# Kernel tuning notes

Hardware: AMD Instinct MI355X
Metric: run time of the kernel (lower is better)

## Reference

```python
import jax, jax.numpy as jnp
import numpy as np

B, T, C = 4, 2048, 1024
H = 16
HS = C // H  # 64
FF = 4 * C  # 4096


def setup_inputs() -> dict:
    key = jax.random.key(0)
    ks = jax.random.split(key, 10)
    s_in = C ** -0.5
    s_ff = FF ** -0.5
    return {
        "x": jax.random.normal(ks[0], (B, T, C), dtype=jnp.float32),
        "Wq": jax.random.normal(ks[1], (H, C, HS), dtype=jnp.float32) * s_in,
        "Wk": jax.random.normal(ks[2], (H, C, HS), dtype=jnp.float32) * s_in,
        "Wv": jax.random.normal(ks[3], (H, C, HS), dtype=jnp.float32) * s_in,
        "Wproj": jax.random.normal(ks[4], (C, C), dtype=jnp.float32) * s_in,
        "bproj": jax.random.normal(ks[5], (C,), dtype=jnp.float32) * 0.01,
        "W1": jax.random.normal(ks[6], (C, FF), dtype=jnp.float32) * s_in,
        "b1": jax.random.normal(ks[7], (FF,), dtype=jnp.float32) * 0.01,
        "W2": jax.random.normal(ks[8], (FF, C), dtype=jnp.float32) * s_ff,
        "b2": jax.random.normal(ks[9], (C,), dtype=jnp.float32) * 0.01,
    }


def reference(x, Wq, Wk, Wv, Wproj, bproj, W1, b1, W2, b2):
    b, t, c = x.shape
    # per-head projections, batched over heads: [B,H,T,HS]
    q = jnp.einsum("btc,hcd->bhtd", x, Wq)
    k = jnp.einsum("btc,hcd->bhtd", x, Wk)
    v = jnp.einsum("btc,hcd->bhtd", x, Wv)
    # NOTE: original scales by full embed dim c**-0.5, not head_size
    scores = jnp.einsum("bhtd,bhsd->bhts", q, k) * (c ** -0.5)
    causal = jnp.tril(jnp.ones((t, t), dtype=bool))
    scores = jnp.where(causal[None, None], scores, -jnp.inf)
    w = jax.nn.softmax(scores, axis=-1)
    y = jnp.einsum("bhts,bhsd->bhtd", w, v)  # [B,H,T,HS]
    y = jnp.transpose(y, (0, 2, 1, 3)).reshape(b, t, c)  # concat heads
    attn_out = y @ Wproj + bproj
    x = attn_out + x
    ff = jax.nn.relu(x @ W1 + b1) @ W2 + b2
    return ff + x
```

## Files before the change

### kernel.cpp

```cpp
#include <hip/hip_runtime.h>

typedef unsigned short u16;
typedef __attribute__((ext_vector_type(4))) float f32x4;
typedef __attribute__((ext_vector_type(8))) short bf16x8;

constexpr int kB  = 4;
constexpr int kT  = 2048;
constexpr int kC  = 1024;
constexpr int kH  = 16;
constexpr int kFF = 4096;
constexpr int kM  = kB * kT;
constexpr int k3C = 3 * kC;

__device__ __forceinline__ float b2f(u16 u) {
    union { unsigned int i; float f; } v;
    v.i = ((unsigned int)u) << 16;
    return v.f;
}
__device__ __forceinline__ u16 f2b(float f) {
    union { float f; unsigned int i; } v;
    v.f = f;
    unsigned int r = (v.i + 0x7FFFu + ((v.i >> 16) & 1u)) >> 16;
    return (u16)r;
}

__device__ __forceinline__ void lds_barrier() {
    __asm__ __volatile__("" ::: "memory");
    __builtin_amdgcn_s_waitcnt(0xC07F);
    __builtin_amdgcn_s_barrier();
    __asm__ __volatile__("" ::: "memory");
}

__global__ void cvt_f32_bf16(const float* __restrict__ in, u16* __restrict__ out, int n4)
{
    const int i = blockIdx.x * 256 + threadIdx.x;
    if (i >= n4) return;
    float4 v = *(const float4*)(in + (size_t)i * 4);
    ushort4 o;
    o.x = f2b(v.x); o.y = f2b(v.y); o.z = f2b(v.z); o.w = f2b(v.w);
    *(ushort4*)(out + (size_t)i * 4) = o;
}

__global__ void transpose_cvt(const float* __restrict__ in, int R, int Cc,
                              u16* __restrict__ out)
{
    __shared__ float t[32][33];
    const int bx = blockIdx.x * 32;
    const int by = blockIdx.y * 32;
    const int lx = threadIdx.x, ly = threadIdx.y;
    #pragma unroll
    for (int i = 0; i < 32; i += 8)
        t[ly + i][lx] = in[(size_t)(by + ly + i) * Cc + bx + lx];
    __syncthreads();
    #pragma unroll
    for (int i = 0; i < 32; i += 8)
        out[(size_t)(bx + ly + i) * R + by + lx] = f2b(t[lx][ly + i]);
}

__global__ void repack_qkv_t(const float* __restrict__ Wq, const float* __restrict__ Wk,
                             const float* __restrict__ Wv, u16* __restrict__ out)
{
    __shared__ float t[32][33];
    const int z = blockIdx.z;
    const int s = z >> 4, h = z & 15;
    const float* in = (s == 0 ? Wq : s == 1 ? Wk : Wv) + (size_t)h * (kC * 64);
    const int bx = blockIdx.x * 32;
    const int by = blockIdx.y * 32;
    const int lx = threadIdx.x, ly = threadIdx.y;
    #pragma unroll
    for (int i = 0; i < 32; i += 8)
        t[ly + i][lx] = in[(size_t)(by + ly + i) * 64 + bx + lx];
    __syncthreads();
    const int orow = s * kC + h * 64 + bx;
    #pragma unroll
    for (int i = 0; i < 32; i += 8)
        out[(size_t)(orow + ly + i) * kC + by + lx] = f2b(t[lx][ly + i]);
}

__global__ __launch_bounds__(256) void gemm_bt_mfma(
    const u16* __restrict__ A, int lda,
    const u16* __restrict__ Bt, int ldb,
    int K,
    const float* __restrict__ bias,
    const u16* __restrict__ resid,
    float* __restrict__ CoF,
    u16* __restrict__ CoB,
    int ldc, int do_relu)
{
    constexpr int BK = 64;
    __shared__ u16 As[128 * BK];
    __shared__ u16 Bs[128 * BK];
    const int tid  = threadIdx.x;
    const int wave = tid >> 6, lane = tid & 63;
    const int wm = (wave >> 1) * 64, wn = (wave & 1) * 64;
    const int m0 = blockIdx.y * 128, n0 = blockIdx.x * 128;

    const int srow = wave * 32;
    const int lrow = lane >> 3;
    const int scol = ((lane & 7) ^ lrow) * 8;

    const int fm   = lane & 15;
    const int fkq  = lane >> 4;

    f32x4 acc[4][4];
    #pragma unroll
    for (int i = 0; i < 4; ++i)
        #pragma unroll
        for (int j = 0; j < 4; ++j)
            acc[i][j] = (f32x4){0.f, 0.f, 0.f, 0.f};

    for (int k0 = 0; k0 < K; k0 += BK) {
        #pragma unroll
        for (int i = 0; i < 4; ++i) {
            const int r = srow + i * 8;
            const u16* ga = A  + (size_t)(m0 + r + lrow) * lda + k0 + scol;
            const u16* gb = Bt + (size_t)(n0 + r + lrow) * ldb + k0 + scol;
            __builtin_amdgcn_global_load_lds(
                (const __attribute__((address_space(1))) void*)ga,
                (__attribute__((address_space(3))) void*)&As[r * BK], 16, 0, 0);
            __builtin_amdgcn_global_load_lds(
                (const __attribute__((address_space(1))) void*)gb,
                (__attribute__((address_space(3))) void*)&Bs[r * BK], 16, 0, 0);
        }
        __syncthreads();
        #pragma unroll
        for (int ks = 0; ks < 2; ++ks) {
            bf16x8 a[4], b[4];
            #pragma unroll
            for (int i = 0; i < 4; ++i) {
                const int m = wm + i * 16 + fm;
                const int ck = ((ks * 4 + fkq) ^ (m & 7)) * 8;
                a[i] = *(const bf16x8*)&As[m * BK + ck];
            }
            #pragma unroll
            for (int j = 0; j < 4; ++j) {
                const int n = wn + j * 16 + fm;
                const int ck = ((ks * 4 + fkq) ^ (n & 7)) * 8;
                b[j] = *(const bf16x8*)&Bs[n * BK + ck];
            }
            #pragma unroll
            for (int i = 0; i < 4; ++i)
                #pragma unroll
                for (int j = 0; j < 4; ++j)
                    acc[i][j] = __builtin_amdgcn_mfma_f32_16x16x32_bf16(
                        a[i], b[j], acc[i][j], 0, 0, 0);
        }
        __syncthreads();
    }

    const int col = lane & 15;
    const int rb  = (lane >> 4) * 4;
    #pragma unroll
    for (int i = 0; i < 4; ++i) {
        #pragma unroll
        for (int j = 0; j < 4; ++j) {
            const int n = n0 + wn + j * 16 + col;
            #pragma unroll
            for (int r = 0; r < 4; ++r) {
                const int m = m0 + wm + i * 16 + rb + r;
                float v = acc[i][j][r];
                if (bias)    v += bias[n];
                if (do_relu) v = fmaxf(v, 0.f);
                if (resid)   v += b2f(resid[(size_t)m * ldc + n]);
                if (CoF) CoF[(size_t)m * ldc + n] = v;
                else     CoB[(size_t)m * ldc + n] = f2b(v);
            }
        }
    }
}

__global__ __launch_bounds__(256) void attn_mfma3(
    const u16* __restrict__ QKV, u16* __restrict__ Y)
{
    __shared__ __align__(16) u16 Kl[2][64 * 64];
    __shared__ __align__(16) u16 Vt[2][64 * 64];
    __shared__ __align__(16) u16 Pl[4][16 * 64];

    const int tid  = threadIdx.x;
    const int wave = tid >> 6, lane = tid & 63;
    const int ln = lane & 15, quad = lane >> 4;
    const int idx = blockIdx.x;
    const int bh = idx & 63;
    const int qt = 15 - (idx >> 6);
    const int b = bh >> 4, h = bh & 15;
    const int q0 = qt << 7;
    const int bT = b * kT;
    const int qgw = q0 + wave * 32;
    const float scale = 0.03125f;

    const u16* kvbase = QKV + (size_t)bT * k3C + kC + h * 64;

    const int sK = tid >> 3, cK = tid & 7;
    const int sV = (tid >> 3) * 2, cV = tid & 7;
    const int kwa0 = (sK << 6) + ((cK ^ (sK & 7)) << 3);
    const int kwa1 = kwa0 + (32 << 6);

    bf16x8 qa[2][2];
    #pragma unroll
    for (int qsub = 0; qsub < 2; ++qsub) {
        const size_t qb = ((size_t)bT + qgw + 16 * qsub + ln) * k3C + h * 64;
        qa[qsub][0] = *(const bf16x8*)(QKV + qb + quad * 8);
        qa[qsub][1] = *(const bf16x8*)(QKV + qb + 32 + quad * 8);
    }

    f32x4 acco[2][4];
    #pragma unroll
    for (int qsub = 0; qsub < 2; ++qsub)
        #pragma unroll
        for (int jd = 0; jd < 4; ++jd) acco[qsub][jd] = (f32x4){0.f, 0.f, 0.f, 0.f};
    float mrun[2] = {-1e30f, -1e30f}, lrun[2] = {0.f, 0.f};
    u16* Pw = Pl[wave];

    const int ntiles = 2 * qt + 2;

    auto loadkv = [&](int s0p, uint4& k0, uint4& k1, uint4& v0, uint4& v1) {
        const u16* kg = kvbase + (size_t)(s0p + sK) * k3C + cK * 8;
        k0 = *(const uint4*)kg;
        k1 = *(const uint4*)(kg + (size_t)32 * k3C);
        const u16* vg = kvbase + kC + (size_t)(s0p + sV) * k3C + cV * 8;
        v0 = *(const uint4*)vg;
        v1 = *(const uint4*)(vg + k3C);
    };
    auto stage = [&](u16* Kb, u16* Vb, const uint4& k0, const uint4& k1,
                     const uint4& v0, const uint4& v1) {
        *(uint4*)&Kb[kwa0] = k0;
        *(uint4*)&Kb[kwa1] = k1;
        const u16* t0 = (const u16*)&v0;
        const u16* t1 = (const u16*)&v1;
        #pragma unroll
        for (int i = 0; i < 8; ++i) {
            const int d = cV * 8 + i;
            const int chunk = ((sV >> 3) ^ (d & 7) ^ ((d >> 3) & 7)) & 7;
            ushort2 pr; pr.x = t0[i]; pr.y = t1[i];
            *(ushort2*)&Vb[(d << 6) + (chunk << 3) + (sV & 7)] = pr;
        }
    };
    auto compute = [&](int t, const u16* Kb, const u16* Vb) {
        const int s0 = t << 6;
        if (s0 > qgw + 31) return;
        f32x4 accs[2][4];
        #pragma unroll
        for (int qsub = 0; qsub < 2; ++qsub)
            #pragma unroll
            for (int j = 0; j < 4; ++j) accs[qsub][j] = (f32x4){0.f, 0.f, 0.f, 0.f};
        #pragma unroll
        for (int ks = 0; ks < 2; ++ks) {
            #pragma unroll
            for (int j = 0; j < 4; ++j) {
                const int s = j * 16 + ln;
                bf16x8 kb = *(const bf16x8*)&Kb[(s << 6) + ((((quad + 4 * ks) ^ (s & 7)) & 7) << 3)];
                accs[0][j] = __builtin_amdgcn_mfma_f32_16x16x32_bf16(kb, qa[0][ks], accs[0][j], 0, 0, 0);
                accs[1][j] = __builtin_amdgcn_mfma_f32_16x16x32_bf16(kb, qa[1][ks], accs[1][j], 0, 0, 0);
            }
        }
        bf16x8 vfr[4][2];
        #pragma unroll
        for (int jd = 0; jd < 4; ++jd) {
            const int d = jd * 16 + ln;
            #pragma unroll
            for (int ks = 0; ks < 2; ++ks)
                vfr[jd][ks] = *(const bf16x8*)&Vb[(d << 6) + ((((quad + 4 * ks) ^ (d & 7) ^ ((d >> 3) & 7)) & 7) << 3)];
        }
        #pragma unroll
        for (int qsub = 0; qsub < 2; ++qsub) {
            const int qg = qgw + 16 * qsub + ln;
            float part = -1e30f;
            #pragma unroll
            for (int j = 0; j < 4; ++j) {
                #pragma unroll
                for (int r = 0; r < 4; ++r) {
                    const int sg = s0 + j * 16 + quad * 4 + r;
                    float v = accs[qsub][j][r] * scale;
                    v = (sg <= qg) ? v : -1e30f;
                    accs[qsub][j][r] = v;
                    part = fmaxf(part, v);
                }
            }
            float mx = fmaxf(part, __shfl_xor(part, 16));
            mx = fmaxf(mx, __shfl_xor(mx, 32));
            const float mn = fmaxf(mrun[qsub], mx);
            const float al = __expf(mrun[qsub] - mn);
            mrun[qsub] = mn;
            float ls = 0.f;
            #pragma unroll
            for (int j = 0; j < 4; ++j)
                #pragma unroll
                for (int r = 0; r < 4; ++r) {
                    const float p = __expf(accs[qsub][j][r] - mn);
                    accs[qsub][j][r] = p;
                    ls += p;
                }
            ls += __shfl_xor(ls, 16);
            ls += __shfl_xor(ls, 32);
            lrun[qsub] = lrun[qsub] * al + ls;
            #pragma unroll
            for (int jd = 0; jd < 4; ++jd)
                #pragma unroll
                for (int r = 0; r < 4; ++r)
                    acco[qsub][jd][r] *= al;
            #pragma unroll
            for (int j = 0; j < 4; ++j) {
                ushort4 pk;
                pk.x = f2b(accs[qsub][j][0]); pk.y = f2b(accs[qsub][j][1]);
                pk.z = f2b(accs[qsub][j][2]); pk.w = f2b(accs[qsub][j][3]);
                const int chunk = ((2 * j + (quad >> 1)) ^ (ln & 7)) & 7;
                *(ushort4*)&Pw[(ln << 6) + (chunk << 3) + ((quad & 1) << 2)] = pk;
            }
            #pragma unroll
            for (int ks = 0; ks < 2; ++ks) {
                bf16x8 pb = *(const bf16x8*)&Pw[(ln << 6) + ((((4 * ks + quad) ^ (ln & 7)) & 7) << 3)];
                #pragma unroll
                for (int jd = 0; jd < 4; ++jd)
                    acco[qsub][jd] = __builtin_amdgcn_mfma_f32_16x16x32_bf16(
                        vfr[jd][ks], pb, acco[qsub][jd], 0, 0, 0);
            }
        }
    };

    uint4 ka0, ka1, va0, va1, kb0, kb1, vb0, vb1;
    loadkv(0, ka0, ka1, va0, va1);
    for (int t = 0; t < ntiles; t += 2) {
        stage(Kl[0], Vt[0], ka0, ka1, va0, va1);
        loadkv((t + 1) << 6, kb0, kb1, vb0, vb1);
        lds_barrier();
        compute(t, Kl[0], Vt[0]);
        stage(Kl[1], Vt[1], kb0, kb1, vb0, vb1);
        loadkv(((t + 2) < ntiles ? (t + 2) : 0) << 6, ka0, ka1, va0, va1);
        lds_barrier();
        compute(t + 1, Kl[1], Vt[1]);
    }

    #pragma unroll
    for (int qsub = 0; qsub < 2; ++qsub) {
        const float inv = 1.f / lrun[qsub];
        const size_t yrow = ((size_t)bT + qgw + 16 * qsub + ln) * kC + h * 64;
        #pragma unroll
        for (int jd = 0; jd < 4; ++jd) {
            ushort4 ov;
            ov.x = f2b(acco[qsub][jd][0] * inv);
            ov.y = f2b(acco[qsub][jd][1] * inv);
            ov.z = f2b(acco[qsub][jd][2] * inv);
            ov.w = f2b(acco[qsub][jd][3] * inv);
            *(ushort4*)(Y + yrow + jd * 16 + quad * 4) = ov;
        }
    }
}

extern "C" void kernel_launch(void* const* d_in, const int* in_sizes, int n_in,
                              void* d_out, int out_size, void* d_ws, size_t ws_size,
                              hipStream_t stream) {
    const float* x     = (const float*)d_in[0];
    const float* Wq    = (const float*)d_in[1];
    const float* Wk    = (const float*)d_in[2];
    const float* Wv    = (const float*)d_in[3];
    const float* Wproj = (const float*)d_in[4];
    const float* bproj = (const float*)d_in[5];
    const float* W1    = (const float*)d_in[6];
    const float* b1    = (const float*)d_in[7];
    const float* W2    = (const float*)d_in[8];
    const float* b2    = (const float*)d_in[9];

    u16* ws      = (u16*)d_ws;
    u16* QKV     = ws;
    u16* ffh     = ws;
    u16* attn_y  = ws + (size_t)kM * kFF;
    u16* xb      = attn_y  + (size_t)kM * kC;
    u16* res1    = xb      + (size_t)kM * kC;
    u16* Wqkv_t  = res1    + (size_t)kM * kC;
    u16* Wproj_t = Wqkv_t  + (size_t)k3C * kC;
    u16* W1t     = Wproj_t + (size_t)kC * kC;
    u16* W2t     = W1t     + (size_t)kFF * kC;
    float* out   = (float*)d_out;

    cvt_f32_bf16<<<(kM * kC / 4 + 255) / 256, 256, 0, stream>>>(x, xb, kM * kC / 4);
    repack_qkv_t<<<dim3(2, kC / 32, 48), dim3(32, 8), 0, stream>>>(Wq, Wk, Wv, Wqkv_t);
    transpose_cvt<<<dim3(kC / 32, kC / 32),  dim3(32, 8), 0, stream>>>(Wproj, kC, kC, Wproj_t);
    transpose_cvt<<<dim3(kFF / 32, kC / 32), dim3(32, 8), 0, stream>>>(W1, kC, kFF, W1t);
    transpose_cvt<<<dim3(kC / 32, kFF / 32), dim3(32, 8), 0, stream>>>(W2, kFF, kC, W2t);

    gemm_bt_mfma<<<dim3(k3C / 128, kM / 128), 256, 0, stream>>>(
        xb, kC, Wqkv_t, kC, kC, nullptr, nullptr, nullptr, QKV, k3C, 0);
    attn_mfma3<<<dim3(1024), 256, 0, stream>>>(QKV, attn_y);
    gemm_bt_mfma<<<dim3(kC / 128, kM / 128), 256, 0, stream>>>(
        attn_y, kC, Wproj_t, kC, kC, bproj, xb, nullptr, res1, kC, 0);
    gemm_bt_mfma<<<dim3(kFF / 128, kM / 128), 256, 0, stream>>>(
        res1, kC, W1t, kC, kC, b1, nullptr, nullptr, ffh, kFF, 1);
    gemm_bt_mfma<<<dim3(kC / 128, kM / 128), 256, 0, stream>>>(
        ffh, kFF, W2t, kFF, kFF, b2, res1, out, nullptr, kC, 0);
}
```

Baseline: 609.8 us.

## Prefetch next GEMM K-tile into registers to overlap loads with MFMA

The GEMM main loop no longer loads global tiles directly into LDS and then waits. It now prefetches the next K-tile into registers while the MFMAs on the current tile run. The registers are written to LDS at the start of each iteration between two LDS barriers, and the trailing __syncthreads is removed. This hides global memory latency inside each block, at the cost of extra VGPRs for the staging buffers, extra LDS store instructions, and possibly lower occupancy.

```diff
diff --git a/kernel.cpp b/kernel.cpp
--- a/kernel.cpp
+++ b/kernel.cpp
@@ -98,6 +98,7 @@
     const int srow = wave * 32;
     const int lrow = lane >> 3;
     const int scol = ((lane & 7) ^ lrow) * 8;
+    const int wcol = (lane & 7) * 8;
 
     const int fm   = lane & 15;
     const int fkq  = lane >> 4;
@@ -109,20 +110,34 @@
         for (int j = 0; j < 4; ++j)
             acc[i][j] = (f32x4){0.f, 0.f, 0.f, 0.f};
 
-    for (int k0 = 0; k0 < K; k0 += BK) {
+    const u16* ap = A  + (size_t)(m0 + srow + lrow) * lda + scol;
+    const u16* bp = Bt + (size_t)(n0 + srow + lrow) * ldb + scol;
+
+    uint4 ra[4], rb[4];
+    #pragma unroll
+    for (int i = 0; i < 4; ++i) {
+        ra[i] = *(const uint4*)(ap + (size_t)(i * 8) * lda);
+        rb[i] = *(const uint4*)(bp + (size_t)(i * 8) * ldb);
+    }
+
+    const int nt = K / BK;
+    for (int t = 0; t < nt; ++t) {
+        lds_barrier();
         #pragma unroll
         for (int i = 0; i < 4; ++i) {
-            const int r = srow + i * 8;
-            const u16* ga = A  + (size_t)(m0 + r + lrow) * lda + k0 + scol;
-            const u16* gb = Bt + (size_t)(n0 + r + lrow) * ldb + k0 + scol;
-            __builtin_amdgcn_global_load_lds(
-                (const __attribute__((address_space(1))) void*)ga,
-                (__attribute__((address_space(3))) void*)&As[r * BK], 16, 0, 0);
-            __builtin_amdgcn_global_load_lds(
-                (const __attribute__((address_space(1))) void*)gb,
-                (__attribute__((address_space(3))) void*)&Bs[r * BK], 16, 0, 0);
-        }
-        __syncthreads();
+            const int r = srow + i * 8 + lrow;
+            *(uint4*)&As[r * BK + wcol] = ra[i];
+            *(uint4*)&Bs[r * BK + wcol] = rb[i];
+        }
+        if (t + 1 < nt) {
+            const int k0 = (t + 1) * BK;
+            #pragma unroll
+            for (int i = 0; i < 4; ++i) {
+                ra[i] = *(const uint4*)(ap + (size_t)(i * 8) * lda + k0);
+                rb[i] = *(const uint4*)(bp + (size_t)(i * 8) * ldb + k0);
+            }
+        }
+        lds_barrier();
         #pragma unroll
         for (int ks = 0; ks < 2; ++ks) {
             bf16x8 a[4], b[4];
@@ -145,11 +160,10 @@
                     acc[i][j] = __builtin_amdgcn_mfma_f32_16x16x32_bf16(
                         a[i], b[j], acc[i][j], 0, 0, 0);
         }
-        __syncthreads();
     }
 
     const int col = lane & 15;
-    const int rb  = (lane >> 4) * 4;
+    const int rb2 = (lane >> 4) * 4;
     #pragma unroll
     for (int i = 0; i < 4; ++i) {
         #pragma unroll
@@ -157,7 +171,7 @@
             const int n = n0 + wn + j * 16 + col;
             #pragma unroll
             for (int r = 0; r < 4; ++r) {
-                const int m = m0 + wm + i * 16 + rb + r;
+                const int m = m0 + wm + i * 16 + rb2 + r;
                 float v = acc[i][j][r];
                 if (bias)    v += bias[n];
                 if (do_relu) v = fmaxf(v, 0.f);
```

Result: slower. 1.170 ms (+91.9%).
